# Optimization experiments

Measured on AMD Instinct MI355X. Metric: run time of the kernel, lower is better.

The kernel has to match this reference:

```python
import jax, jax.numpy as jnp
import numpy as np
from jax import lax

PS = 8  # patch size

def setup_inputs() -> dict:
    key = jax.random.key(0)
    ks = jax.random.split(key, 7)
    dim = 64
    B, H, W = 4, 256, 256
    x = jax.random.normal(ks[0], (B, dim, H, W), dtype=jnp.float32)
    # to_hidden: Conv2d(dim, 6*dim, k=1)
    w_hidden = jax.random.normal(ks[1], (6 * dim, dim, 1, 1), dtype=jnp.float32) * 0.05
    b_hidden = jax.random.normal(ks[2], (6 * dim,), dtype=jnp.float32) * 0.01
    # to_hidden_dw: depthwise Conv2d(6*dim, 6*dim, k=3, pad=1, groups=6*dim)
    w_dw = jax.random.normal(ks[3], (6 * dim, 1, 3, 3), dtype=jnp.float32) * 0.05
    b_dw = jax.random.normal(ks[4], (6 * dim,), dtype=jnp.float32) * 0.01
    # project_out: Conv2d(2*dim, dim, k=1)
    w_out = jax.random.normal(ks[5], (dim, 2 * dim, 1, 1), dtype=jnp.float32) * 0.05
    b_out = jax.random.normal(ks[6], (dim,), dtype=jnp.float32) * 0.01
    return {"x": x, "w_hidden": w_hidden, "b_hidden": b_hidden,
            "w_dw": w_dw, "b_dw": b_dw, "w_out": w_out, "b_out": b_out}

def _conv(x, w, groups=1, padding='VALID'):
    return lax.conv_general_dilated(
        x, w, window_strides=(1, 1), padding=padding,
        dimension_numbers=('NCHW', 'OIHW', 'NCHW'),
        feature_group_count=groups)

def reference(x, w_hidden, b_hidden, w_dw, b_dw, w_out, b_out):
    # 1x1 expansion to 6*dim channels
    hidden = _conv(x, w_hidden) + b_hidden[None, :, None, None]
    # 3x3 depthwise conv (groups == channels)
    dw = _conv(hidden, w_dw, groups=w_dw.shape[0], padding='SAME') + b_dw[None, :, None, None]
    q, k, v = jnp.split(dw, 3, axis=1)  # each (B, 2*dim, H, W)
    B, C, H, W = q.shape
    # raw reshape into (B,C,H/8,W/8,8,8) exactly as torch .reshape on contiguous NCHW
    q_patch = q.reshape(B, C, H // PS, W // PS, PS, PS)
    k_patch = k.reshape(B, C, H // PS, W // PS, PS, PS)
    q_fft = jnp.fft.rfft2(q_patch)
    k_fft = jnp.fft.rfft2(k_patch)
    out = jnp.fft.irfft2(q_fft * k_fft, s=(PS, PS))  # circular conv of q,k patches
    out = out.reshape(B, C, (H // PS) * PS, (W // PS) * PS)
    output = v * out
    output = _conv(output, w_out) + b_out[None, :, None, None]
    return output
```

## Files before the change

kernel.cpp:

```cpp
#include <hip/hip_runtime.h>

#define HW 65536
#define W_IMG 256
#define H_IMG 256
#define CIN 64
#define CHID 384
#define CQK 128

__global__ __launch_bounds__(256) void k1_expand(
    const float* __restrict__ x_base,
    const float* __restrict__ wh,
    const float* __restrict__ bh,
    float* __restrict__ hidden_base,
    size_t x_bstride, size_t hid_bstride)
{
    const float* x = x_base + blockIdx.z * x_bstride;
    float* hidden  = hidden_base + blockIdx.z * hid_bstride;
    const int pxbase = blockIdx.x * 256;
    const int cobase = blockIdx.y * 48;
    const int tid  = threadIdx.x;
    const int lane = tid & 63;
    const int wq   = __builtin_amdgcn_readfirstlane(tid >> 6);
    const int px   = pxbase + lane * 4;

    #pragma unroll
    for (int st = 0; st < 2; ++st) {
        const int cw = cobase + st * 24 + wq * 6;
        float acc[6][4];
        #pragma unroll
        for (int i = 0; i < 6; ++i)
            #pragma unroll
            for (int j = 0; j < 4; ++j) acc[i][j] = 0.f;

        #pragma unroll 2
        for (int ci4 = 0; ci4 < CIN; ci4 += 4) {
            float4 xv[4];
            #pragma unroll
            for (int u = 0; u < 4; ++u)
                xv[u] = *reinterpret_cast<const float4*>(&x[(size_t)(ci4 + u) * HW + px]);
            #pragma unroll
            for (int i = 0; i < 6; ++i) {
                float4 wv = *reinterpret_cast<const float4*>(
                    &wh[(size_t)(cw + i) * CIN + ci4]);
                float wu[4] = {wv.x, wv.y, wv.z, wv.w};
                #pragma unroll
                for (int u = 0; u < 4; ++u) {
                    acc[i][0] += wu[u] * xv[u].x;
                    acc[i][1] += wu[u] * xv[u].y;
                    acc[i][2] += wu[u] * xv[u].z;
                    acc[i][3] += wu[u] * xv[u].w;
                }
            }
        }

        #pragma unroll
        for (int i = 0; i < 6; ++i) {
            int co = cw + i;
            float b = bh[co];
            float4 o;
            o.x = acc[i][0] + b; o.y = acc[i][1] + b;
            o.z = acc[i][2] + b; o.w = acc[i][3] + b;
            *reinterpret_cast<float4*>(&hidden[(size_t)co * HW + px]) = o;
        }
    }
}

#define QK_CH   2208
#define QK_ROW  276
#define QK_SEG  68
__global__ __launch_bounds__(256) void k2_fused(
    const float* __restrict__ hidden_base,
    const float* __restrict__ wdw,
    const float* __restrict__ bdw,
    float* __restrict__ vout_base,
    size_t hid_bstride, size_t vout_bstride)
{
    __shared__ float stg[10 * 264];
    __shared__ float qk[2 * QK_CH];

    const float* hidden = hidden_base + blockIdx.z * hid_bstride;
    float* vout         = vout_base + blockIdx.z * vout_bstride;

    const int c  = blockIdx.y;
    const int r0 = blockIdx.x * 8;
    const int tid = threadIdx.x;

    const int row = tid >> 5;
    const int seg = (tid >> 3) & 3;
    const int i   = tid & 7;
    const int gr  = r0 + row;
    const int wp0 = seg * 64 + i * 8;

    float4 qreg[3];
    #pragma unroll
    for (int it = 0; it < 3; ++it) {
        int f4 = it * 256 + tid;
        qreg[it] = make_float4(0.f, 0.f, 0.f, 0.f);
        if (f4 < 640) {
            int lr = f4 >> 6, p4 = f4 & 63;
            int grr = r0 - 1 + lr;
            if ((unsigned)grr < H_IMG)
                qreg[it] = *reinterpret_cast<const float4*>(
                    &hidden[(size_t)c * HW + (size_t)grr * W_IMG + p4 * 4]);
        }
    }
    float4 kreg[3];
    #pragma unroll
    for (int it = 0; it < 3; ++it) {
        int f4 = it * 256 + tid;
        kreg[it] = make_float4(0.f, 0.f, 0.f, 0.f);
        if (f4 < 640) {
            int lr = f4 >> 6, p4 = f4 & 63;
            int grr = r0 - 1 + lr;
            if ((unsigned)grr < H_IMG)
                kreg[it] = *reinterpret_cast<const float4*>(
                    &hidden[(size_t)(c + CQK) * HW + (size_t)grr * W_IMG + p4 * 4]);
        }
    }

    #pragma unroll
    for (int it = 0; it < 3; ++it) {
        int f4 = it * 256 + tid;
        if (f4 < 640) {
            int lr = f4 >> 6, p4 = f4 & 63;
            *reinterpret_cast<float4*>(&stg[lr * 264 + 4 + p4 * 4]) = qreg[it];
        }
    }
    if (tid < 10) {
        stg[tid * 264 + 3]   = 0.f;
        stg[tid * 264 + 260] = 0.f;
    }

    const float* hbv = hidden + (size_t)(c + 2 * CQK) * HW;
    float4 hv[3][2];
    float  hm[3], hp[3];
    #pragma unroll
    for (int ky = 0; ky < 3; ++ky) {
        int grr = gr + ky - 1;
        hv[ky][0] = make_float4(0.f, 0.f, 0.f, 0.f);
        hv[ky][1] = make_float4(0.f, 0.f, 0.f, 0.f);
        hm[ky] = 0.f; hp[ky] = 0.f;
        if ((unsigned)grr < H_IMG) {
            const float* rb = hbv + (size_t)grr * W_IMG;
            hv[ky][0] = *reinterpret_cast<const float4*>(&rb[wp0]);
            hv[ky][1] = *reinterpret_cast<const float4*>(&rb[wp0 + 4]);
            hm[ky] = (wp0 > 0)   ? rb[wp0 - 1] : 0.f;
            hp[ky] = (wp0 < 248) ? rb[wp0 + 8] : 0.f;
        }
    }

    const int w = tid;
    const int segw = w >> 6;
    const int tw   = w & 63;

    #pragma unroll
    for (int ch = 0; ch < 2; ++ch) {
        if (ch) {
            __syncthreads();
            #pragma unroll
            for (int it = 0; it < 3; ++it) {
                int f4 = it * 256 + tid;
                if (f4 < 640) {
                    int lr = f4 >> 6, p4 = f4 & 63;
                    *reinterpret_cast<float4*>(&stg[lr * 264 + 4 + p4 * 4]) = kreg[it];
                }
            }
        }
        __syncthreads();

        const float* wv = wdw + (c + ch * CQK) * 9;
        const float bias = bdw[c + ch * CQK];
        const float w0 = wv[0], w1 = wv[1], w2 = wv[2];
        const float w3 = wv[3], w4 = wv[4], w5 = wv[5];
        const float w6 = wv[6], w7 = wv[7], w8 = wv[8];

        const float* S0 = &stg[w + 3];
        float am = S0[0],   a0 = S0[1],   ap = S0[2];
        float bm = S0[264], b0 = S0[265], bp = S0[266];
        #pragma unroll
        for (int r = 0; r < 8; ++r) {
            const float* Sr = S0 + (r + 2) * 264;
            float cm = Sr[0], c0 = Sr[1], cp = Sr[2];
            float a = bias + am * w0 + a0 * w1 + ap * w2
                           + bm * w3 + b0 * w4 + bp * w5
                           + cm * w6 + c0 * w7 + cp * w8;
            qk[ch * QK_CH + r * QK_ROW + segw * QK_SEG + tw] = a;
            am = bm; a0 = b0; ap = bp;
            bm = cm; b0 = c0; bp = cp;
        }
    }
    __syncthreads();

    const float* qb = &qk[row * QK_ROW + seg * QK_SEG];
    const float* kb = &qk[QK_CH + row * QK_ROW + seg * QK_SEG];

    float acc[8];
    #pragma unroll
    for (int j = 0; j < 8; ++j) acc[j] = 0.f;

    #pragma unroll
    for (int s = 0; s < 8; ++s) {
        int qr = (i - s) & 7;
        float4 ka = *reinterpret_cast<const float4*>(&kb[s * 8]);
        float4 kc = *reinterpret_cast<const float4*>(&kb[s * 8 + 4]);
        float4 qa = *reinterpret_cast<const float4*>(&qb[qr * 8]);
        float4 qc = *reinterpret_cast<const float4*>(&qb[qr * 8 + 4]);
        float kr[8] = {ka.x, ka.y, ka.z, ka.w, kc.x, kc.y, kc.z, kc.w};
        float qv[8] = {qa.x, qa.y, qa.z, qa.w, qc.x, qc.y, qc.z, qc.w};
        #pragma unroll
        for (int t = 0; t < 8; ++t)
            #pragma unroll
            for (int j = 0; j < 8; ++j)
                acc[j] += kr[t] * qv[(j - t) & 7];
    }

    const float* wvv = wdw + (c + 2 * CQK) * 9;
    const float vbias = bdw[c + 2 * CQK];
    float vc[8];
    #pragma unroll
    for (int j = 0; j < 8; ++j) vc[j] = vbias;
    #pragma unroll
    for (int ky = 0; ky < 3; ++ky) {
        float kw0 = wvv[ky * 3], kw1 = wvv[ky * 3 + 1], kw2 = wvv[ky * 3 + 2];
        float h[10];
        h[0] = hm[ky];
        h[1] = hv[ky][0].x; h[2] = hv[ky][0].y; h[3] = hv[ky][0].z; h[4] = hv[ky][0].w;
        h[5] = hv[ky][1].x; h[6] = hv[ky][1].y; h[7] = hv[ky][1].z; h[8] = hv[ky][1].w;
        h[9] = hp[ky];
        #pragma unroll
        for (int j = 0; j < 8; ++j)
            vc[j] += h[j] * kw0 + h[j + 1] * kw1 + h[j + 2] * kw2;
    }

    float* dst = &vout[(size_t)c * HW + (size_t)gr * W_IMG + wp0];
    float4 o0, o1;
    o0.x = acc[0] * vc[0]; o0.y = acc[1] * vc[1];
    o0.z = acc[2] * vc[2]; o0.w = acc[3] * vc[3];
    o1.x = acc[4] * vc[4]; o1.y = acc[5] * vc[5];
    o1.z = acc[6] * vc[6]; o1.w = acc[7] * vc[7];
    *reinterpret_cast<float4*>(dst)     = o0;
    *reinterpret_cast<float4*>(dst + 4) = o1;
}

__global__ __launch_bounds__(256) void k3_project(
    const float* __restrict__ vout_base,
    const float* __restrict__ wo,
    const float* __restrict__ bo,
    float* __restrict__ out_base,
    size_t vout_bstride, size_t out_bstride)
{
    const float* vout = vout_base + blockIdx.z * vout_bstride;
    float* out        = out_base + blockIdx.z * out_bstride;
    const int pxbase = blockIdx.x * 256;
    const int cobase = blockIdx.y * 16;
    const int tid  = threadIdx.x;
    const int lane = tid & 63;
    const int wq   = __builtin_amdgcn_readfirstlane(tid >> 6);
    const int px   = pxbase + lane * 4;
    const int cw   = cobase + wq * 4;

    float acc[4][4];
    #pragma unroll
    for (int i = 0; i < 4; ++i)
        #pragma unroll
        for (int j = 0; j < 4; ++j) acc[i][j] = 0.f;

    #pragma unroll 2
    for (int cc4 = 0; cc4 < CQK; cc4 += 4) {
        float4 xv[4];
        #pragma unroll
        for (int u = 0; u < 4; ++u)
            xv[u] = *reinterpret_cast<const float4*>(&vout[(size_t)(cc4 + u) * HW + px]);
        #pragma unroll
        for (int i = 0; i < 4; ++i) {
            float4 wv = *reinterpret_cast<const float4*>(
                &wo[(size_t)(cw + i) * CQK + cc4]);
            float wu[4] = {wv.x, wv.y, wv.z, wv.w};
            #pragma unroll
            for (int u = 0; u < 4; ++u) {
                acc[i][0] += wu[u] * xv[u].x;
                acc[i][1] += wu[u] * xv[u].y;
                acc[i][2] += wu[u] * xv[u].z;
                acc[i][3] += wu[u] * xv[u].w;
            }
        }
    }

    #pragma unroll
    for (int i = 0; i < 4; ++i) {
        int co = cw + i;
        float b = bo[co];
        float4 o;
        o.x = acc[i][0] + b; o.y = acc[i][1] + b;
        o.z = acc[i][2] + b; o.w = acc[i][3] + b;
        *reinterpret_cast<float4*>(&out[(size_t)co * HW + px]) = o;
    }
}

extern "C" void kernel_launch(void* const* d_in, const int* in_sizes, int n_in,
                              void* d_out, int out_size, void* d_ws, size_t ws_size,
                              hipStream_t stream) {
    const float* x   = (const float*)d_in[0];
    const float* wh  = (const float*)d_in[1];
    const float* bh  = (const float*)d_in[2];
    const float* wdw = (const float*)d_in[3];
    const float* bdw = (const float*)d_in[4];
    const float* wo  = (const float*)d_in[5];
    const float* bo  = (const float*)d_in[6];
    float* out = (float*)d_out;

    const size_t n_hid  = (size_t)CHID * HW;
    const size_t n_vout = (size_t)CQK * HW;
    const size_t n_x    = (size_t)CIN * HW;

    if (ws_size >= 4 * (n_hid + n_vout) * sizeof(float)) {
        float* hidden = (float*)d_ws;
        float* vout   = hidden + 4 * n_hid;
        k1_expand <<<dim3(HW / 256, CHID / 48, 4), 256, 0, stream>>>(
            x, wh, bh, hidden, n_x, n_hid);
        k2_fused  <<<dim3(H_IMG / 8, CQK, 4),      256, 0, stream>>>(
            hidden, wdw, bdw, vout, n_hid, n_vout);
        k3_project<<<dim3(HW / 256, 64 / 16, 4),   256, 0, stream>>>(
            vout, wo, bo, out, n_vout, n_x);
    } else {
        float* hidden = (float*)d_ws;
        float* vout   = hidden + n_hid;
        for (int b = 0; b < 4; ++b) {
            const float* xb = x + (size_t)b * n_x;
            float* ob       = out + (size_t)b * n_x;
            k1_expand <<<dim3(HW / 256, CHID / 48, 1), 256, 0, stream>>>(
                xb, wh, bh, hidden, 0, 0);
            k2_fused  <<<dim3(H_IMG / 8, CQK, 1),      256, 0, stream>>>(
                hidden, wdw, bdw, vout, 0, 0);
            k3_project<<<dim3(HW / 256, 64 / 16, 1),   256, 0, stream>>>(
                vout, wo, bo, ob, 0, 0);
        }
    }
}
```

Baseline: 432.6 us.

## Double-buffer input loads in 1x1 convs and stage q/k in separate LDS buffers

The expansion kernel now computes 12 output channels per wave in a single pass instead of two passes of 6. This removes the second read of the x inputs. Both 1x1 conv kernels prefetch the next group of four input channels into registers while the current group is being accumulated, so global load latency can hide behind the FMAs. The fused depthwise kernel stages q and k into two separate shared buffers at once, which removes one barrier and the serialized k staging. In exchange, register use (48 accumulators) and LDS use both go up, which may lower occupancy.

```diff
diff --git a/kernel.cpp b/kernel.cpp
--- a/kernel.cpp
+++ b/kernel.cpp
@@ -22,46 +22,65 @@
     const int lane = tid & 63;
     const int wq   = __builtin_amdgcn_readfirstlane(tid >> 6);
     const int px   = pxbase + lane * 4;
-
-    #pragma unroll
-    for (int st = 0; st < 2; ++st) {
-        const int cw = cobase + st * 24 + wq * 6;
-        float acc[6][4];
-        #pragma unroll
-        for (int i = 0; i < 6; ++i)
-            #pragma unroll
-            for (int j = 0; j < 4; ++j) acc[i][j] = 0.f;
-
-        #pragma unroll 2
-        for (int ci4 = 0; ci4 < CIN; ci4 += 4) {
-            float4 xv[4];
+    const int cw   = cobase + wq * 12;
+
+    float acc[12][4];
+    #pragma unroll
+    for (int i = 0; i < 12; ++i)
+        #pragma unroll
+        for (int j = 0; j < 4; ++j) acc[i][j] = 0.f;
+
+    float4 xa[4], xb[4];
+    #pragma unroll
+    for (int u = 0; u < 4; ++u)
+        xa[u] = *reinterpret_cast<const float4*>(&x[(size_t)u * HW + px]);
+
+    #pragma unroll 1
+    for (int ci4 = 0; ci4 < CIN; ci4 += 8) {
+        #pragma unroll
+        for (int u = 0; u < 4; ++u)
+            xb[u] = *reinterpret_cast<const float4*>(&x[(size_t)(ci4 + 4 + u) * HW + px]);
+        #pragma unroll
+        for (int i = 0; i < 12; ++i) {
+            float4 wv = *reinterpret_cast<const float4*>(
+                &wh[(size_t)(cw + i) * CIN + ci4]);
+            float wu[4] = {wv.x, wv.y, wv.z, wv.w};
+            #pragma unroll
+            for (int u = 0; u < 4; ++u) {
+                acc[i][0] += wu[u] * xa[u].x;
+                acc[i][1] += wu[u] * xa[u].y;
+                acc[i][2] += wu[u] * xa[u].z;
+                acc[i][3] += wu[u] * xa[u].w;
+            }
+        }
+        if (ci4 + 8 < CIN) {
             #pragma unroll
             for (int u = 0; u < 4; ++u)
-                xv[u] = *reinterpret_cast<const float4*>(&x[(size_t)(ci4 + u) * HW + px]);
-            #pragma unroll
-            for (int i = 0; i < 6; ++i) {
-                float4 wv = *reinterpret_cast<const float4*>(
-                    &wh[(size_t)(cw + i) * CIN + ci4]);
-                float wu[4] = {wv.x, wv.y, wv.z, wv.w};
-                #pragma unroll
-                for (int u = 0; u < 4; ++u) {
-                    acc[i][0] += wu[u] * xv[u].x;
-                    acc[i][1] += wu[u] * xv[u].y;
-                    acc[i][2] += wu[u] * xv[u].z;
-                    acc[i][3] += wu[u] * xv[u].w;
-                }
+                xa[u] = *reinterpret_cast<const float4*>(&x[(size_t)(ci4 + 8 + u) * HW + px]);
+        }
+        #pragma unroll
+        for (int i = 0; i < 12; ++i) {
+            float4 wv = *reinterpret_cast<const float4*>(
+                &wh[(size_t)(cw + i) * CIN + ci4 + 4]);
+            float wu[4] = {wv.x, wv.y, wv.z, wv.w};
+            #pragma unroll
+            for (int u = 0; u < 4; ++u) {
+                acc[i][0] += wu[u] * xb[u].x;
+                acc[i][1] += wu[u] * xb[u].y;
+                acc[i][2] += wu[u] * xb[u].z;
+                acc[i][3] += wu[u] * xb[u].w;
             }
         }
-
-        #pragma unroll
-        for (int i = 0; i < 6; ++i) {
-            int co = cw + i;
-            float b = bh[co];
-            float4 o;
-            o.x = acc[i][0] + b; o.y = acc[i][1] + b;
-            o.z = acc[i][2] + b; o.w = acc[i][3] + b;
-            *reinterpret_cast<float4*>(&hidden[(size_t)co * HW + px]) = o;
-        }
+    }
+
+    #pragma unroll
+    for (int i = 0; i < 12; ++i) {
+        int co = cw + i;
+        float b = bh[co];
+        float4 o;
+        o.x = acc[i][0] + b; o.y = acc[i][1] + b;
+        o.z = acc[i][2] + b; o.w = acc[i][3] + b;
+        *reinterpret_cast<float4*>(&hidden[(size_t)co * HW + px]) = o;
     }
 }
 
@@ -75,7 +94,8 @@
     float* __restrict__ vout_base,
     size_t hid_bstride, size_t vout_bstride)
 {
-    __shared__ float stg[10 * 264];
+    __shared__ float stgq[10 * 264];
+    __shared__ float stgk[10 * 264];
     __shared__ float qk[2 * QK_CH];
 
     const float* hidden = hidden_base + blockIdx.z * hid_bstride;
@@ -91,7 +111,7 @@
     const int gr  = r0 + row;
     const int wp0 = seg * 64 + i * 8;
 
-    float4 qreg[3];
+    float4 qreg[3], kreg[3];
     #pragma unroll
     for (int it = 0; it < 3; ++it) {
         int f4 = it * 256 + tid;
@@ -104,7 +124,6 @@
                     &hidden[(size_t)c * HW + (size_t)grr * W_IMG + p4 * 4]);
         }
     }
-    float4 kreg[3];
     #pragma unroll
     for (int it = 0; it < 3; ++it) {
         int f4 = it * 256 + tid;
@@ -123,12 +142,15 @@
         int f4 = it * 256 + tid;
         if (f4 < 640) {
             int lr = f4 >> 6, p4 = f4 & 63;
-            *reinterpret_cast<float4*>(&stg[lr * 264 + 4 + p4 * 4]) = qreg[it];
+            *reinterpret_cast<float4*>(&stgq[lr * 264 + 4 + p4 * 4]) = qreg[it];
+            *reinterpret_cast<float4*>(&stgk[lr * 264 + 4 + p4 * 4]) = kreg[it];
         }
     }
     if (tid < 10) {
-        stg[tid * 264 + 3]   = 0.f;
-        stg[tid * 264 + 260] = 0.f;
+        stgq[tid * 264 + 3]   = 0.f;
+        stgq[tid * 264 + 260] = 0.f;
+        stgk[tid * 264 + 3]   = 0.f;
+        stgk[tid * 264 + 260] = 0.f;
     }
 
     const float* hbv = hidden + (size_t)(c + 2 * CQK) * HW;
@@ -149,32 +171,22 @@
         }
     }
 
+    __syncthreads();
+
     const int w = tid;
     const int segw = w >> 6;
     const int tw   = w & 63;
 
     #pragma unroll
     for (int ch = 0; ch < 2; ++ch) {
-        if (ch) {
-            __syncthreads();
-            #pragma unroll
-            for (int it = 0; it < 3; ++it) {
-                int f4 = it * 256 + tid;
-                if (f4 < 640) {
-                    int lr = f4 >> 6, p4 = f4 & 63;
-                    *reinterpret_cast<float4*>(&stg[lr * 264 + 4 + p4 * 4]) = kreg[it];
-                }
-            }
-        }
-        __syncthreads();
-
+        const float* S = ch ? stgk : stgq;
         const float* wv = wdw + (c + ch * CQK) * 9;
         const float bias = bdw[c + ch * CQK];
         const float w0 = wv[0], w1 = wv[1], w2 = wv[2];
         const float w3 = wv[3], w4 = wv[4], w5 = wv[5];
         const float w6 = wv[6], w7 = wv[7], w8 = wv[8];
 
-        const float* S0 = &stg[w + 3];
+        const float* S0 = S + w + 3;
         float am = S0[0],   a0 = S0[1],   ap = S0[2];
         float bm = S0[264], b0 = S0[265], bp = S0[266];
         #pragma unroll
@@ -265,12 +277,16 @@
         #pragma unroll
         for (int j = 0; j < 4; ++j) acc[i][j] = 0.f;
 
-    #pragma unroll 2
-    for (int cc4 = 0; cc4 < CQK; cc4 += 4) {
-        float4 xv[4];
+    float4 xa[4], xb[4];
+    #pragma unroll
+    for (int u = 0; u < 4; ++u)
+        xa[u] = *reinterpret_cast<const float4*>(&vout[(size_t)u * HW + px]);
+
+    #pragma unroll 1
+    for (int cc4 = 0; cc4 < CQK; cc4 += 8) {
         #pragma unroll
         for (int u = 0; u < 4; ++u)
-            xv[u] = *reinterpret_cast<const float4*>(&vout[(size_t)(cc4 + u) * HW + px]);
+            xb[u] = *reinterpret_cast<const float4*>(&vout[(size_t)(cc4 + 4 + u) * HW + px]);
         #pragma unroll
         for (int i = 0; i < 4; ++i) {
             float4 wv = *reinterpret_cast<const float4*>(
@@ -278,10 +294,28 @@
             float wu[4] = {wv.x, wv.y, wv.z, wv.w};
             #pragma unroll
             for (int u = 0; u < 4; ++u) {
-                acc[i][0] += wu[u] * xv[u].x;
-                acc[i][1] += wu[u] * xv[u].y;
-                acc[i][2] += wu[u] * xv[u].z;
-                acc[i][3] += wu[u] * xv[u].w;
+                acc[i][0] += wu[u] * xa[u].x;
+                acc[i][1] += wu[u] * xa[u].y;
+                acc[i][2] += wu[u] * xa[u].z;
+                acc[i][3] += wu[u] * xa[u].w;
+            }
+        }
+        if (cc4 + 8 < CQK) {
+            #pragma unroll
+            for (int u = 0; u < 4; ++u)
+                xa[u] = *reinterpret_cast<const float4*>(&vout[(size_t)(cc4 + 8 + u) * HW + px]);
+        }
+        #pragma unroll
+        for (int i = 0; i < 4; ++i) {
+            float4 wv = *reinterpret_cast<const float4*>(
+                &wo[(size_t)(cw + i) * CQK + cc4 + 4]);
+            float wu[4] = {wv.x, wv.y, wv.z, wv.w};
+            #pragma unroll
+            for (int u = 0; u < 4; ++u) {
+                acc[i][0] += wu[u] * xb[u].x;
+                acc[i][1] += wu[u] * xb[u].y;
+                acc[i][2] += wu[u] * xb[u].z;
+                acc[i][3] += wu[u] * xb[u].w;
             }
         }
     }
```

Result: faster. 398.9 us (-7.8%).
